# Kernel optimization log

Measured on AMD Instinct MI355X. Metric: run time of the kernel, lower is better.

The kernel has to match this reference:

```python
import jax, jax.numpy as jnp
import numpy as np
import math

B, S, H, NH, NB = 2, 512, 128, 4, 2
D = H // NH
V_ITEMS, NCAT, NMETA, BAG, TSPAN = 50000, 1000, 16, 5, 256
EPS_EMB, EPS = 1e-5, 1e-8
NEG = -(2.0 ** 32) + 1.0


def _ln(x, g, b, eps):
    m = x.mean(-1, keepdims=True)
    v = ((x - m) ** 2).mean(-1, keepdims=True)
    return (x - m) / jnp.sqrt(v + eps) * g + b


def setup_inputs() -> dict:
    key = jax.random.key(0)
    ks = jax.random.split(key, 24)
    sc = 0.02
    inp = {}
    inp['input_ids'] = jax.random.randint(ks[0], (B, S), 0, V_ITEMS + 1)
    inp['metadata_seq'] = jax.random.normal(ks[1], (B, S, NMETA), jnp.float32)
    inp['category_seq'] = jax.random.randint(ks[2], (B, S, BAG), 0, NCAT + 1)
    inp['time_matrix'] = jax.random.randint(ks[3], (B, S, S), 0, TSPAN + 1)
    item = jax.random.normal(ks[4], (V_ITEMS + 1, H), jnp.float32) * sc
    inp['item_emb_w'] = item.at[0].set(0.0)  # padding_idx=0 cleared
    cat = jax.random.normal(ks[5], (NCAT + 1, H // 2), jnp.float32) * sc
    inp['cat_emb_w'] = cat.at[0].set(0.0)
    inp['num_W'] = jax.random.normal(ks[6], (H // 2, NMETA), jnp.float32) * sc
    inp['num_b'] = jnp.zeros((H // 2,), jnp.float32)
    inp['fusion_W'] = jax.random.normal(ks[7], (H, 2 * H), jnp.float32) * sc
    inp['fusion_b'] = jnp.zeros((H,), jnp.float32)
    inp['emb_ln_g'] = jnp.ones((H,), jnp.float32)
    inp['emb_ln_b'] = jnp.zeros((H,), jnp.float32)
    inp['pos_K_w'] = jax.random.normal(ks[8], (S, H), jnp.float32) * sc
    inp['pos_V_w'] = jax.random.normal(ks[9], (S, H), jnp.float32) * sc
    inp['time_K_w'] = jax.random.normal(ks[10], (TSPAN + 1, H), jnp.float32) * sc
    inp['time_V_w'] = jax.random.normal(ks[11], (TSPAN + 1, H), jnp.float32) * sc
    inp['attn_ln_g'] = jnp.ones((NB, H), jnp.float32)
    inp['attn_ln_b'] = jnp.zeros((NB, H), jnp.float32)
    inp['Q_W'] = jax.random.normal(ks[12], (NB, H, H), jnp.float32) * sc
    inp['Q_b'] = jnp.zeros((NB, H), jnp.float32)
    inp['K_W'] = jax.random.normal(ks[13], (NB, H, H), jnp.float32) * sc
    inp['K_b'] = jnp.zeros((NB, H), jnp.float32)
    inp['V_W'] = jax.random.normal(ks[14], (NB, H, H), jnp.float32) * sc
    inp['V_b'] = jnp.zeros((NB, H), jnp.float32)
    inp['fwd_ln_g'] = jnp.ones((NB, H), jnp.float32)
    inp['fwd_ln_b'] = jnp.zeros((NB, H), jnp.float32)
    inp['w1_W'] = jax.random.normal(ks[15], (NB, H, H), jnp.float32) * sc
    inp['w1_b'] = jnp.zeros((NB, H), jnp.float32)
    inp['w2_W'] = jax.random.normal(ks[16], (NB, H, H), jnp.float32) * sc
    inp['w2_b'] = jnp.zeros((NB, H), jnp.float32)
    inp['last_ln_g'] = jnp.ones((H,), jnp.float32)
    inp['last_ln_b'] = jnp.zeros((H,), jnp.float32)
    return inp


def reference(input_ids, metadata_seq, category_seq, time_matrix, item_emb_w,
              cat_emb_w, num_W, num_b, fusion_W, fusion_b, emb_ln_g, emb_ln_b,
              pos_K_w, pos_V_w, time_K_w, time_V_w, attn_ln_g, attn_ln_b,
              Q_W, Q_b, K_W, K_b, V_W, V_b, fwd_ln_g, fwd_ln_b,
              w1_W, w1_b, w2_W, w2_b, last_ln_g, last_ln_b):
    # ---- seq2vec ----
    item_v = item_emb_w[input_ids] * math.sqrt(H)            # [B,S,H]
    bag_mask = (category_seq != 0)                           # EmbeddingBag mean, padding_idx=0
    cat_e = cat_emb_w[category_seq] * bag_mask[..., None]    # [B,S,BAG,H/2]
    cat_v = cat_e.sum(-2) / jnp.maximum(bag_mask.sum(-1, keepdims=True), 1)
    num_v = metadata_seq @ num_W.T + num_b                   # [B,S,H/2]
    comb = jnp.concatenate([item_v, num_v, cat_v], axis=-1)  # [B,S,2H]
    vecs = _ln(comb @ fusion_W.T + fusion_b, emb_ln_g, emb_ln_b, EPS_EMB)

    # ---- vec2feats ----
    posK = pos_K_w.reshape(S, NH, D)
    posV = pos_V_w.reshape(S, NH, D)
    tK = time_K_w[time_matrix].reshape(B, S, S, NH, D)       # [B,S,S,h,d]
    tV = time_V_w[time_matrix].reshape(B, S, S, NH, D)
    timeline = (input_ids == 0)                              # [B,S]
    keep = (~timeline)[..., None].astype(vecs.dtype)
    vecs = vecs * keep
    causal = ~jnp.tril(jnp.ones((S, S), bool))               # mask where j > i
    inv_sqrt_d = 1.0 / math.sqrt(D)

    for i in range(NB):
        Qn = _ln(vecs, attn_ln_g[i], attn_ln_b[i], EPS)
        Q = (Qn @ Q_W[i].T + Q_b[i]).reshape(B, S, NH, D)
        K = (vecs @ K_W[i].T + K_b[i]).reshape(B, S, NH, D)
        V = (vecs @ V_W[i].T + V_b[i]).reshape(B, S, NH, D)
        aw = jnp.einsum('bihd,bjhd->bhij', Q, K)
        aw = aw + jnp.einsum('bihd,jhd->bhij', Q, posK)
        aw = aw + jnp.einsum('bijhd,bihd->bhij', tK, Q)
        aw = aw * inv_sqrt_d
        aw = jnp.where(timeline[:, None, :, None], NEG, aw)  # masks query rows (as in torch)
        aw = jnp.where(causal[None, None], NEG, aw)
        aw = jax.nn.softmax(aw, axis=-1)
        out = jnp.einsum('bhij,bjhd->bihd', aw, V)
        out = out + jnp.einsum('bhij,jhd->bihd', aw, posV)
        out = out + jnp.einsum('bhij,bijhd->bihd', aw, tV)
        out = out.reshape(B, S, H)
        vecs = Qn + out
        vecs = _ln(vecs, fwd_ln_g[i], fwd_ln_b[i], EPS)
        h1 = jax.nn.gelu(vecs @ w1_W[i].T + w1_b[i], approximate=False)
        vecs = vecs + (h1 @ w2_W[i].T + w2_b[i])
        vecs = vecs * keep

    return _ln(vecs, last_ln_g, last_ln_b, EPS)
```

## Files before the change

kernel.cpp:

```cpp
#include <hip/hip_runtime.h>
#include <math.h>

#define Bn 2
#define Sn 512
#define Hn 128
#define NHn 4
#define Dn 32
#define BAGn 5
#define NMETAn 16
#define ROWS 1024
#define NBn 2
#define Tt 257

#define NEGF (-4294967295.0f)
#define INV_SQRT_D 0.17677669529663687f
#define SQRT_H 11.313708498984761f
#define EPS_EMB 1e-5f
#define EPSF 1e-8f

#define OFF_QN    0
#define OFF_Q     131072
#define OFF_K     262144
#define OFF_V     393216
#define OFF_O     524288

static __device__ __forceinline__ float red64(float v) {
#pragma unroll
    for (int m = 1; m < 64; m <<= 1) v += __shfl_xor(v, m, 64);
    return v;
}
static __device__ __forceinline__ float red64max(float v) {
#pragma unroll
    for (int m = 1; m < 64; m <<= 1) v = fmaxf(v, __shfl_xor(v, m, 64));
    return v;
}

__global__ __launch_bounds__(256) void embed_qkv_kernel(
    const int* __restrict__ ids, const float* __restrict__ meta,
    const int* __restrict__ cats,
    const float* __restrict__ item_w, const float* __restrict__ cat_w,
    const float* __restrict__ numW, const float* __restrict__ numb,
    const float* __restrict__ fusW, const float* __restrict__ fusb,
    const float* __restrict__ elng, const float* __restrict__ elnb,
    const float* __restrict__ alng, const float* __restrict__ alnb,
    const float* __restrict__ QW, const float* __restrict__ Qb,
    const float* __restrict__ KW, const float* __restrict__ Kb,
    const float* __restrict__ VW, const float* __restrict__ Vb,
    const float* __restrict__ posK, const float* __restrict__ posV,
    float* __restrict__ Qn, float* __restrict__ Q,
    float* __restrict__ K, float* __restrict__ V)
{
    int r0 = blockIdx.x * 2, t = threadIdx.x;
    __shared__ float combs[512], xs[256], qs[256], parts[256], pk[256], pv[256];
    __shared__ float wsum[8];
    __shared__ int idl[2];
    if (t < 2) idl[t] = ids[r0 + t];
    __syncthreads();
    { int r = t >> 7, c = t & 127; combs[r * 256 + c] = item_w[idl[r] * Hn + c] * SQRT_H; }
    if (t < 128) {
        int r = t >> 6, c = t & 63;
        float acc = numb[c];
#pragma unroll
        for (int m2 = 0; m2 < NMETAn; ++m2)
            acc += meta[(r0 + r) * NMETAn + m2] * numW[c * NMETAn + m2];
        combs[r * 256 + 128 + c] = acc;
    } else {
        int u = t - 128, r = u >> 6, c = u & 63;
        float ca = 0.f; int cnt = 0;
#pragma unroll
        for (int k2 = 0; k2 < BAGn; ++k2) {
            int cc2 = cats[(r0 + r) * BAGn + k2];
            if (cc2 != 0) { ca += cat_w[cc2 * 64 + c]; cnt++; }
        }
        combs[r * 256 + 192 + c] = ca / (float)(cnt > 0 ? cnt : 1);
    }
    __syncthreads();
    int h = t & 127, kh = t >> 7;
    {
        const float4* w4p = (const float4*)(fusW + h * 256 + kh * 128);
        const float* c0 = combs + kh * 128;
        const float* c1 = combs + 256 + kh * 128;
        float a0 = 0.f, a1 = 0.f, b0 = 0.f, b1 = 0.f;
#pragma unroll 16
        for (int k4 = 0; k4 < 32; ++k4) {
            float4 w4 = w4p[k4];
            int k = k4 * 4;
            a0 += c0[k] * w4.x + c0[k + 1] * w4.y;
            a1 += c0[k + 2] * w4.z + c0[k + 3] * w4.w;
            b0 += c1[k] * w4.x + c1[k + 1] * w4.y;
            b1 += c1[k + 2] * w4.z + c1[k + 3] * w4.w;
        }
        float A0 = a0 + a1, A1 = b0 + b1;
        if (kh) { parts[h] = A0; parts[128 + h] = A1; }
        __syncthreads();
        if (!kh) {
            xs[h] = A0 + parts[h] + fusb[h];
            xs[128 + h] = A1 + parts[128 + h] + fusb[h];
        }
    }
    __syncthreads();
    int w_ = t >> 6, row = w_ >> 1, l = t & 63, ch = ((w_ & 1) << 6) + l;
    float x = xs[row * 128 + ch];
    float s1 = red64(x);
    if (l == 0) wsum[w_] = s1;
    __syncthreads();
    float mean = (wsum[row * 2] + wsum[row * 2 + 1]) * (1.f / 128.f);
    float dlt = x - mean;
    float s2 = red64(dlt * dlt);
    if (l == 0) wsum[4 + w_] = s2;
    __syncthreads();
    float rstd = rsqrtf((wsum[4 + row * 2] + wsum[4 + row * 2 + 1]) * (1.f / 128.f) + EPS_EMB);
    float xv = dlt * rstd * elng[ch] + elnb[ch];
    xv = (idl[row] == 0) ? 0.f : xv;
    __syncthreads();
    xs[row * 128 + ch] = xv;
    __syncthreads();
    s1 = red64(xv);
    if (l == 0) wsum[w_] = s1;
    __syncthreads();
    mean = (wsum[row * 2] + wsum[row * 2 + 1]) * (1.f / 128.f);
    dlt = xv - mean;
    s2 = red64(dlt * dlt);
    if (l == 0) wsum[4 + w_] = s2;
    __syncthreads();
    rstd = rsqrtf((wsum[4 + row * 2] + wsum[4 + row * 2 + 1]) * (1.f / 128.f) + EPSF);
    float qn = dlt * rstd * alng[ch] + alnb[ch];
    qs[row * 128 + ch] = qn;
    Qn[(r0 + row) * 128 + ch] = qn;
    __syncthreads();
    {
        const float4* qw4 = (const float4*)(QW + h * 128 + kh * 64);
        const float4* kw4 = (const float4*)(KW + h * 128 + kh * 64);
        const float4* vw4 = (const float4*)(VW + h * 128 + kh * 64);
        const float* q0p = qs + kh * 64;
        const float* q1p = qs + 128 + kh * 64;
        const float* x0p = xs + kh * 64;
        const float* x1p = xs + 128 + kh * 64;
        float aq0 = 0, aq1 = 0, ak0 = 0, ak1 = 0, av0 = 0, av1 = 0;
#pragma unroll 8
        for (int k4 = 0; k4 < 16; ++k4) {
            float4 wq = qw4[k4], wk = kw4[k4], wv = vw4[k4];
            int k = k4 * 4;
            aq0 += q0p[k] * wq.x + q0p[k + 1] * wq.y + q0p[k + 2] * wq.z + q0p[k + 3] * wq.w;
            aq1 += q1p[k] * wq.x + q1p[k + 1] * wq.y + q1p[k + 2] * wq.z + q1p[k + 3] * wq.w;
            ak0 += x0p[k] * wk.x + x0p[k + 1] * wk.y + x0p[k + 2] * wk.z + x0p[k + 3] * wk.w;
            ak1 += x1p[k] * wk.x + x1p[k + 1] * wk.y + x1p[k + 2] * wk.z + x1p[k + 3] * wk.w;
            av0 += x0p[k] * wv.x + x0p[k + 1] * wv.y + x0p[k + 2] * wv.z + x0p[k + 3] * wv.w;
            av1 += x1p[k] * wv.x + x1p[k + 1] * wv.y + x1p[k + 2] * wv.z + x1p[k + 3] * wv.w;
        }
        if (kh) {
            parts[h] = aq0; parts[128 + h] = aq1;
            pk[h] = ak0; pk[128 + h] = ak1;
            pv[h] = av0; pv[128 + h] = av1;
        }
        __syncthreads();
        if (!kh) {
            int s0 = r0 & (Sn - 1), s1_ = (r0 + 1) & (Sn - 1);
            Q[r0 * 128 + h]       = aq0 + parts[h]       + Qb[h];
            Q[(r0 + 1) * 128 + h] = aq1 + parts[128 + h] + Qb[h];
            K[r0 * 128 + h]       = ak0 + pk[h]          + Kb[h] + posK[s0 * 128 + h];
            K[(r0 + 1) * 128 + h] = ak1 + pk[128 + h]    + Kb[h] + posK[s1_ * 128 + h];
            V[r0 * 128 + h]       = av0 + pv[h]          + Vb[h] + posV[s0 * 128 + h];
            V[(r0 + 1) * 128 + h] = av1 + pv[128 + h]    + Vb[h] + posV[s1_ * 128 + h];
        }
    }
}

static __device__ __forceinline__ void attn_phase(
    int b, int h, int i0, int t,
    const int* __restrict__ ids, const int* __restrict__ tmat,
    const float* __restrict__ Q, const float* __restrict__ K,
    const float* __restrict__ V,
    const float* __restrict__ tKw, const float* __restrict__ tVw,
    float* __restrict__ O,
    float* Kt, float* Vt, float* Stile, int* trowT,
    float* QTl, float* ql, int* tlf)
{
    if (t < 4) tlf[t] = (ids[b * Sn + i0 + t] == 0) ? 1 : 0;
    if (t < 128) {
        int q_ = t >> 5, d = t & 31;
        ql[q_ * 33 + d] = Q[(b * Sn + i0 + q_) * Hn + h * 32 + d];
    }
    __syncthreads();

    for (int tt = t; tt < Tt; tt += 256) {
        const float4* tk4 = (const float4*)(tKw + tt * Hn + h * 32);
        float a0 = 0.f, a1 = 0.f, a2 = 0.f, a3 = 0.f;
#pragma unroll
        for (int dv = 0; dv < 8; ++dv) {
            float4 w4 = tk4[dv];
            int d = dv * 4;
            a0 += ql[d] * w4.x + ql[d + 1] * w4.y + ql[d + 2] * w4.z + ql[d + 3] * w4.w;
            a1 += ql[33 + d] * w4.x + ql[34 + d] * w4.y + ql[35 + d] * w4.z + ql[36 + d] * w4.w;
            a2 += ql[66 + d] * w4.x + ql[67 + d] * w4.y + ql[68 + d] * w4.z + ql[69 + d] * w4.w;
            a3 += ql[99 + d] * w4.x + ql[100 + d] * w4.y + ql[101 + d] * w4.z + ql[102 + d] * w4.w;
        }
        QTl[tt] = a0; QTl[260 + tt] = a1; QTl[520 + tt] = a2; QTl[780 + tt] = a3;
    }

    int tl_any = tlf[0] | tlf[1] | tlf[2] | tlf[3];
    int ntiles = tl_any ? 8 : ((i0 + 3) >> 6) + 1;

    int iq = t >> 6, jj = t & 63;
    int i_g = i0 + iq;
    int my_tl = tlf[iq];
    const int* trow = tmat + (b * Sn + i_g) * Sn;

    float qreg[32];
#pragma unroll
    for (int d = 0; d < 32; ++d) qreg[d] = ql[iq * 33 + d];

    int jq = jj >> 5, d = jj & 31;
    float m = -INFINITY, lsum = 0.f, acc = 0.f;

    for (int jt = 0; jt < ntiles; ++jt) {
        int j0 = jt * 64;
        __syncthreads();
        for (int f = t; f < 64 * 8; f += 256) {
            int jl = f >> 3, dv = f & 7;
            const float* src = K + (b * Sn + j0 + jl) * Hn + h * 32 + dv * 4;
            float4 w4 = *(const float4*)src;
            float* kd = &Kt[jl * 33 + dv * 4];
            kd[0] = w4.x; kd[1] = w4.y; kd[2] = w4.z; kd[3] = w4.w;
            float4 v4 = *(const float4*)(V + (b * Sn + j0 + jl) * Hn + h * 32 + dv * 4);
            float* vd = &Vt[jl * 33 + dv * 4];
            vd[0] = v4.x; vd[1] = v4.y; vd[2] = v4.z; vd[3] = v4.w;
        }
        __syncthreads();

        int active = my_tl || (j0 <= i_g);
        if (active) {
            int j = j0 + jj;
            float sv = NEGF;
            int tv = trow[j];
            if (!my_tl && j <= i_g) {
                float a = 0.f;
#pragma unroll
                for (int dd = 0; dd < 32; ++dd)
                    a += qreg[dd] * Kt[jj * 33 + dd];
                sv = (a + QTl[iq * 260 + tv]) * INV_SQRT_D;
            }
            float mt = red64max(sv);
            float mnew = fmaxf(m, mt);
            float alpha = expf(m - mnew);
            float p = expf(sv - mnew);
            lsum = lsum * alpha + red64(p);
            m = mnew;
            acc *= alpha;
            Stile[iq * 64 + jj] = p;
            trowT[iq * 64 + jj] = tv;
        }
        __syncthreads();
        if (active) {
            int base = jq * 32;
#pragma unroll 8
            for (int jl = base; jl < base + 32; ++jl) {
                float pp = Stile[iq * 64 + jl];
                int tv2 = trowT[iq * 64 + jl];
                acc += pp * (Vt[jl * 33 + d] + tVw[tv2 * Hn + h * 32 + d]);
            }
        }
    }

    float a2 = acc + __shfl_xor(acc, 32, 64);
    if (jj < 32)
        O[(b * Sn + i_g) * Hn + h * 32 + d] = a2 / lsum;
}

__global__ __launch_bounds__(256) void attn_kernel(
    const int* ids, const int* tmat,
    const float* Q, const float* K, const float* V,
    const float* tKw, const float* tVw, float* O)
{
    __shared__ float Kt[64 * 33];
    __shared__ float Vt[64 * 33];
    __shared__ float Stile[4 * 64];
    __shared__ int   trowT[4 * 64];
    __shared__ float QTl[4 * 260];
    __shared__ float ql[4 * 33];
    __shared__ int tlf[4];
    int blk = blockIdx.x, t = threadIdx.x;
    int bh = blk & 7;
    int s  = blk >> 3;
    int g = s >> 5, r = s & 31;
    int m;
    if      (g == 0) m = r;
    else if (g == 1) m = 127 - r;
    else if (g == 2) m = 32 + r;
    else             m = 95 - r;
    int b = bh >> 2, h = bh & 3;
    attn_phase(b, h, m * 4, t, ids, tmat, Q, K, V, tKw, tVw, O,
               Kt, Vt, Stile, trowT, QTl, ql, tlf);
}

__global__ __launch_bounds__(256) void ffn_qkv_kernel(
    const int* __restrict__ ids, float* __restrict__ Qn,
    const float* __restrict__ O,
    const float* __restrict__ flng, const float* __restrict__ flnb,
    const float* __restrict__ w1W, const float* __restrict__ w1b,
    const float* __restrict__ w2W, const float* __restrict__ w2b,
    const float* __restrict__ alng, const float* __restrict__ alnb,
    const float* __restrict__ QW, const float* __restrict__ Qb,
    const float* __restrict__ KW, const float* __restrict__ Kb,
    const float* __restrict__ VW, const float* __restrict__ Vb,
    const float* __restrict__ posK, const float* __restrict__ posV,
    float* __restrict__ Q, float* __restrict__ K, float* __restrict__ V,
    const float* __restrict__ llng, const float* __restrict__ llnb,
    float* __restrict__ out, int nb, int last)
{
    int r0 = blockIdx.x * 2, t = threadIdx.x;
    __shared__ float ys[256], h1s[256], parts[256], pk[256], pv[256];
    __shared__ float wsum[8];
    ys[t] = Qn[r0 * 128 + t] + O[r0 * 128 + t];
    __syncthreads();
    int w_ = t >> 6, row = w_ >> 1, l = t & 63, ch = ((w_ & 1) << 6) + l;
    float x = ys[row * 128 + ch];
    float s1 = red64(x);
    if (l == 0) wsum[w_] = s1;
    __syncthreads();
    float mean = (wsum[row * 2] + wsum[row * 2 + 1]) * (1.f / 128.f);
    float dlt = x - mean;
    float s2 = red64(dlt * dlt);
    if (l == 0) wsum[4 + w_] = s2;
    __syncthreads();
    float rstd = rsqrtf((wsum[4 + row * 2] + wsum[4 + row * 2 + 1]) * (1.f / 128.f) + EPSF);
    float yv = dlt * rstd * flng[nb * 128 + ch] + flnb[nb * 128 + ch];
    __syncthreads();
    ys[row * 128 + ch] = yv;
    __syncthreads();

    int h = t & 127, kh = t >> 7;
    {
        const float4* w4p = (const float4*)(w1W + nb * 16384 + h * 128 + kh * 64);
        const float* y0 = ys + kh * 64;
        const float* y1 = ys + 128 + kh * 64;
        float a0 = 0.f, a1 = 0.f, b0 = 0.f, b1 = 0.f;
#pragma unroll 16
        for (int k4 = 0; k4 < 16; ++k4) {
            float4 w4 = w4p[k4];
            int k = k4 * 4;
            a0 += y0[k] * w4.x + y0[k + 1] * w4.y;
            a1 += y0[k + 2] * w4.z + y0[k + 3] * w4.w;
            b0 += y1[k] * w4.x + y1[k + 1] * w4.y;
            b1 += y1[k + 2] * w4.z + y1[k + 3] * w4.w;
        }
        float A0 = a0 + a1, A1 = b0 + b1;
        if (kh) { parts[h] = A0; parts[128 + h] = A1; }
        __syncthreads();
        if (!kh) {
            float v0 = A0 + parts[h] + w1b[nb * 128 + h];
            float v1 = A1 + parts[128 + h] + w1b[nb * 128 + h];
            h1s[h] = 0.5f * v0 * (1.f + erff(v0 * 0.70710678118654752f));
            h1s[128 + h] = 0.5f * v1 * (1.f + erff(v1 * 0.70710678118654752f));
        }
    }
    __syncthreads();
    {
        const float4* w4p = (const float4*)(w2W + nb * 16384 + h * 128 + kh * 64);
        const float* y0 = h1s + kh * 64;
        const float* y1 = h1s + 128 + kh * 64;
        float a0 = 0.f, a1 = 0.f, b0 = 0.f, b1 = 0.f;
#pragma unroll 16
        for (int k4 = 0; k4 < 16; ++k4) {
            float4 w4 = w4p[k4];
            int k = k4 * 4;
            a0 += y0[k] * w4.x + y0[k + 1] * w4.y;
            a1 += y0[k + 2] * w4.z + y0[k + 3] * w4.w;
            b0 += y1[k] * w4.x + y1[k + 1] * w4.y;
            b1 += y1[k + 2] * w4.z + y1[k + 3] * w4.w;
        }
        float A0 = a0 + a1, A1 = b0 + b1;
        __syncthreads();
        if (kh) { parts[h] = A0; parts[128 + h] = A1; }
        __syncthreads();
        if (!kh) {
            float z0 = A0 + parts[h] + w2b[nb * 128 + h] + ys[h];
            float z1 = A1 + parts[128 + h] + w2b[nb * 128 + h] + ys[128 + h];
            z0 = (ids[r0] == 0) ? 0.f : z0;
            z1 = (ids[r0 + 1] == 0) ? 0.f : z1;
            h1s[h] = z0; h1s[128 + h] = z1;
        }
    }
    __syncthreads();

    if (last) {
        x = h1s[row * 128 + ch];
        s1 = red64(x);
        if (l == 0) wsum[w_] = s1;
        __syncthreads();
        mean = (wsum[row * 2] + wsum[row * 2 + 1]) * (1.f / 128.f);
        dlt = x - mean;
        s2 = red64(dlt * dlt);
        if (l == 0) wsum[4 + w_] = s2;
        __syncthreads();
        rstd = rsqrtf((wsum[4 + row * 2] + wsum[4 + row * 2 + 1]) * (1.f / 128.f) + EPSF);
        out[(r0 + row) * 128 + ch] = dlt * rstd * llng[ch] + llnb[ch];
        return;
    }

    int nq = nb + 1;
    x = h1s[row * 128 + ch];
    s1 = red64(x);
    if (l == 0) wsum[w_] = s1;
    __syncthreads();
    mean = (wsum[row * 2] + wsum[row * 2 + 1]) * (1.f / 128.f);
    dlt = x - mean;
    s2 = red64(dlt * dlt);
    if (l == 0) wsum[4 + w_] = s2;
    __syncthreads();
    rstd = rsqrtf((wsum[4 + row * 2] + wsum[4 + row * 2 + 1]) * (1.f / 128.f) + EPSF);
    float qn = dlt * rstd * alng[nq * 128 + ch] + alnb[nq * 128 + ch];
    __syncthreads();
    ys[row * 128 + ch] = qn;
    Qn[(r0 + row) * 128 + ch] = qn;
    __syncthreads();

    {
        const float4* qw4 = (const float4*)(QW + nq * 16384 + h * 128 + kh * 64);
        const float4* kw4 = (const float4*)(KW + nq * 16384 + h * 128 + kh * 64);
        const float4* vw4 = (const float4*)(VW + nq * 16384 + h * 128 + kh * 64);
        const float* q0p = ys + kh * 64;
        const float* q1p = ys + 128 + kh * 64;
        const float* x0p = h1s + kh * 64;
        const float* x1p = h1s + 128 + kh * 64;
        float aq0 = 0, aq1 = 0, ak0 = 0, ak1 = 0, av0 = 0, av1 = 0;
#pragma unroll 8
        for (int k4 = 0; k4 < 16; ++k4) {
            float4 wq = qw4[k4], wk = kw4[k4], wv = vw4[k4];
            int k = k4 * 4;
            aq0 += q0p[k] * wq.x + q0p[k + 1] * wq.y + q0p[k + 2] * wq.z + q0p[k + 3] * wq.w;
            aq1 += q1p[k] * wq.x + q1p[k + 1] * wq.y + q1p[k + 2] * wq.z + q1p[k + 3] * wq.w;
            ak0 += x0p[k] * wk.x + x0p[k + 1] * wk.y + x0p[k + 2] * wk.z + x0p[k + 3] * wk.w;
            ak1 += x1p[k] * wk.x + x1p[k + 1] * wk.y + x1p[k + 2] * wk.z + x1p[k + 3] * wk.w;
            av0 += x0p[k] * wv.x + x0p[k + 1] * wv.y + x0p[k + 2] * wv.z + x0p[k + 3] * wv.w;
            av1 += x1p[k] * wv.x + x1p[k + 1] * wv.y + x1p[k + 2] * wv.z + x1p[k + 3] * wv.w;
        }
        if (kh) {
            parts[h] = aq0; parts[128 + h] = aq1;
            pk[h] = ak0; pk[128 + h] = ak1;
            pv[h] = av0; pv[128 + h] = av1;
        }
        __syncthreads();
        if (!kh) {
            int s0 = r0 & (Sn - 1), s1_ = (r0 + 1) & (Sn - 1);
            Q[r0 * 128 + h]       = aq0 + parts[h]       + Qb[nq * 128 + h];
            Q[(r0 + 1) * 128 + h] = aq1 + parts[128 + h] + Qb[nq * 128 + h];
            K[r0 * 128 + h]       = ak0 + pk[h]          + Kb[nq * 128 + h] + posK[s0 * 128 + h];
            K[(r0 + 1) * 128 + h] = ak1 + pk[128 + h]    + Kb[nq * 128 + h] + posK[s1_ * 128 + h];
            V[r0 * 128 + h]       = av0 + pv[h]          + Vb[nq * 128 + h] + posV[s0 * 128 + h];
            V[(r0 + 1) * 128 + h] = av1 + pv[128 + h]    + Vb[nq * 128 + h] + posV[s1_ * 128 + h];
        }
    }
}

extern "C" void kernel_launch(void* const* d_in, const int* in_sizes, int n_in,
                              void* d_out, int out_size, void* d_ws, size_t ws_size,
                              hipStream_t stream) {
    const int*   ids   = (const int*)  d_in[0];
    const float* meta  = (const float*)d_in[1];
    const int*   cats  = (const int*)  d_in[2];
    const int*   tmat  = (const int*)  d_in[3];
    const float* itemw = (const float*)d_in[4];
    const float* catw  = (const float*)d_in[5];
    const float* numW  = (const float*)d_in[6];
    const float* numb  = (const float*)d_in[7];
    const float* fusW  = (const float*)d_in[8];
    const float* fusb  = (const float*)d_in[9];
    const float* elng  = (const float*)d_in[10];
    const float* elnb  = (const float*)d_in[11];
    const float* posK  = (const float*)d_in[12];
    const float* posV  = (const float*)d_in[13];
    const float* tKw   = (const float*)d_in[14];
    const float* tVw   = (const float*)d_in[15];
    const float* alng  = (const float*)d_in[16];
    const float* alnb  = (const float*)d_in[17];
    const float* QW    = (const float*)d_in[18];
    const float* Qb    = (const float*)d_in[19];
    const float* KW    = (const float*)d_in[20];
    const float* Kb    = (const float*)d_in[21];
    const float* VW    = (const float*)d_in[22];
    const float* Vb    = (const float*)d_in[23];
    const float* flng  = (const float*)d_in[24];
    const float* flnb  = (const float*)d_in[25];
    const float* w1W   = (const float*)d_in[26];
    const float* w1b   = (const float*)d_in[27];
    const float* w2W   = (const float*)d_in[28];
    const float* w2b   = (const float*)d_in[29];
    const float* llng  = (const float*)d_in[30];
    const float* llnb  = (const float*)d_in[31];
    (void)in_sizes; (void)n_in; (void)out_size; (void)ws_size;

    float* ws = (float*)d_ws;
    float* Qn   = ws + OFF_QN;
    float* Q    = ws + OFF_Q;
    float* K    = ws + OFF_K;
    float* V    = ws + OFF_V;
    float* O    = ws + OFF_O;
    float* out  = (float*)d_out;

    embed_qkv_kernel<<<ROWS / 2, 256, 0, stream>>>(
        ids, meta, cats, itemw, catw, numW, numb, fusW, fusb, elng, elnb,
        alng, alnb, QW, Qb, KW, Kb, VW, Vb, posK, posV, Qn, Q, K, V);
    for (int nb = 0; nb < NBn; ++nb) {
        attn_kernel<<<1024, 256, 0, stream>>>(ids, tmat, Q, K, V, tKw, tVw, O);
        ffn_qkv_kernel<<<ROWS / 2, 256, 0, stream>>>(
            ids, Qn, O, flng, flnb, w1W, w1b, w2W, w2b,
            alng, alnb, QW, Qb, KW, Kb, VW, Vb, posK, posV,
            Q, K, V, llng, llnb, out, nb, (nb == NBn - 1) ? 1 : 0);
    }
}
```

Baseline: 263.7 us.

## Fuse embed, attention and FFN into one cooperative persistent kernel with grid syncs

Replaces the five separate launches (embed, then attention and FFN for each block) with a single cooperative kernel of 512 blocks. The stages are separated by grid-wide syncs, and shared memory is carved out of one buffer that all phases reuse. Each block handles two attention query tiles, pairing tile j with tile 127-j to balance the causal workload. This removes launch gaps and inter-kernel drain at the cost of grid-sync overhead and lower per-phase parallelism for attention (512 blocks instead of 1024). The old multi-kernel path is kept as a fallback when cooperative launch is unavailable.

```diff
diff --git a/kernel.cpp b/kernel.cpp
--- a/kernel.cpp
+++ b/kernel.cpp
@@ -1,5 +1,8 @@
 #include <hip/hip_runtime.h>
+#include <hip/hip_cooperative_groups.h>
 #include <math.h>
+
+namespace cg = cooperative_groups;
 
 #define Bn 2
 #define Sn 512
@@ -35,7 +38,8 @@
     return v;
 }
 
-__global__ __launch_bounds__(256) void embed_qkv_kernel(
+static __device__ __forceinline__ void embed2(
+    int r0, int t, float* sm,
     const int* __restrict__ ids, const float* __restrict__ meta,
     const int* __restrict__ cats,
     const float* __restrict__ item_w, const float* __restrict__ cat_w,
@@ -50,10 +54,15 @@
     float* __restrict__ Qn, float* __restrict__ Q,
     float* __restrict__ K, float* __restrict__ V)
 {
-    int r0 = blockIdx.x * 2, t = threadIdx.x;
-    __shared__ float combs[512], xs[256], qs[256], parts[256], pk[256], pv[256];
-    __shared__ float wsum[8];
-    __shared__ int idl[2];
+    float* combs = sm;
+    float* xs    = sm + 512;
+    float* qs    = sm + 768;
+    float* parts = sm + 1024;
+    float* pk    = sm + 1280;
+    float* pv    = sm + 1536;
+    float* wsum  = sm + 1792;
+    int*   idl   = (int*)(sm + 1800);
+
     if (t < 2) idl[t] = ids[r0 + t];
     __syncthreads();
     { int r = t >> 7, c = t & 127; combs[r * 256 + c] = item_w[idl[r] * Hn + c] * SQRT_H; }
@@ -176,6 +185,7 @@
     float* Kt, float* Vt, float* Stile, int* trowT,
     float* QTl, float* ql, int* tlf)
 {
+    __syncthreads();
     if (t < 4) tlf[t] = (ids[b * Sn + i0 + t] == 0) ? 1 : 0;
     if (t < 128) {
         int q_ = t >> 5, d = t & 31;
@@ -267,33 +277,8 @@
         O[(b * Sn + i_g) * Hn + h * 32 + d] = a2 / lsum;
 }
 
-__global__ __launch_bounds__(256) void attn_kernel(
-    const int* ids, const int* tmat,
-    const float* Q, const float* K, const float* V,
-    const float* tKw, const float* tVw, float* O)
-{
-    __shared__ float Kt[64 * 33];
-    __shared__ float Vt[64 * 33];
-    __shared__ float Stile[4 * 64];
-    __shared__ int   trowT[4 * 64];
-    __shared__ float QTl[4 * 260];
-    __shared__ float ql[4 * 33];
-    __shared__ int tlf[4];
-    int blk = blockIdx.x, t = threadIdx.x;
-    int bh = blk & 7;
-    int s  = blk >> 3;
-    int g = s >> 5, r = s & 31;
-    int m;
-    if      (g == 0) m = r;
-    else if (g == 1) m = 127 - r;
-    else if (g == 2) m = 32 + r;
-    else             m = 95 - r;
-    int b = bh >> 2, h = bh & 3;
-    attn_phase(b, h, m * 4, t, ids, tmat, Q, K, V, tKw, tVw, O,
-               Kt, Vt, Stile, trowT, QTl, ql, tlf);
-}
-
-__global__ __launch_bounds__(256) void ffn_qkv_kernel(
+static __device__ __forceinline__ void ffn2(
+    int r0, int t, float* sm,
     const int* __restrict__ ids, float* __restrict__ Qn,
     const float* __restrict__ O,
     const float* __restrict__ flng, const float* __restrict__ flnb,
@@ -308,9 +293,13 @@
     const float* __restrict__ llng, const float* __restrict__ llnb,
     float* __restrict__ out, int nb, int last)
 {
-    int r0 = blockIdx.x * 2, t = threadIdx.x;
-    __shared__ float ys[256], h1s[256], parts[256], pk[256], pv[256];
-    __shared__ float wsum[8];
+    float* ys    = sm;
+    float* h1s   = sm + 256;
+    float* parts = sm + 512;
+    float* pk    = sm + 768;
+    float* pv    = sm + 1024;
+    float* wsum  = sm + 1280;
+
     ys[t] = Qn[r0 * 128 + t] + O[r0 * 128 + t];
     __syncthreads();
     int w_ = t >> 6, row = w_ >> 1, l = t & 63, ch = ((w_ & 1) << 6) + l;
@@ -452,6 +441,106 @@
         }
     }
 }
+
+__global__ __launch_bounds__(256, 2) void fused_kernel(
+    const int* __restrict__ ids, const float* __restrict__ meta,
+    const int* __restrict__ cats, const int* __restrict__ tmat,
+    const float* __restrict__ item_w, const float* __restrict__ cat_w,
+    const float* __restrict__ numW, const float* __restrict__ numb,
+    const float* __restrict__ fusW, const float* __restrict__ fusb,
+    const float* __restrict__ elng, const float* __restrict__ elnb,
+    const float* __restrict__ posK, const float* __restrict__ posV,
+    const float* __restrict__ tKw, const float* __restrict__ tVw,
+    const float* __restrict__ alng, const float* __restrict__ alnb,
+    const float* __restrict__ QW, const float* __restrict__ Qb,
+    const float* __restrict__ KW, const float* __restrict__ Kb,
+    const float* __restrict__ VW, const float* __restrict__ Vb,
+    const float* __restrict__ flng, const float* __restrict__ flnb,
+    const float* __restrict__ w1W, const float* __restrict__ w1b,
+    const float* __restrict__ w2W, const float* __restrict__ w2b,
+    const float* __restrict__ llng, const float* __restrict__ llnb,
+    float* __restrict__ Qn, float* __restrict__ Q, float* __restrict__ K,
+    float* __restrict__ V, float* __restrict__ O, float* __restrict__ out)
+{
+    cg::grid_group grid = cg::this_grid();
+    __shared__ __align__(16) float sm[5912];
+    int blk = blockIdx.x, t = threadIdx.x;
+    int b8 = blk >> 6, j = blk & 63;
+    int ab = b8 >> 2, ah = b8 & 3;
+
+    embed2(blk * 2, t, sm, ids, meta, cats, item_w, cat_w, numW, numb,
+           fusW, fusb, elng, elnb, alng, alnb, QW, Qb, KW, Kb, VW, Vb,
+           posK, posV, Qn, Q, K, V);
+    grid.sync();
+
+    for (int nb = 0; nb < NBn; ++nb) {
+        attn_phase(ab, ah, j * 4, t, ids, tmat, Q, K, V, tKw, tVw, O,
+                   sm, sm + 2112, sm + 4224, (int*)(sm + 4480),
+                   sm + 4736, sm + 5776, (int*)(sm + 5908));
+        attn_phase(ab, ah, (127 - j) * 4, t, ids, tmat, Q, K, V, tKw, tVw, O,
+                   sm, sm + 2112, sm + 4224, (int*)(sm + 4480),
+                   sm + 4736, sm + 5776, (int*)(sm + 5908));
+        grid.sync();
+        ffn2(blk * 2, t, sm, ids, Qn, O, flng, flnb, w1W, w1b, w2W, w2b,
+             alng, alnb, QW, Qb, KW, Kb, VW, Vb, posK, posV,
+             Q, K, V, llng, llnb, out, nb, (nb == NBn - 1) ? 1 : 0);
+        if (nb == 0) grid.sync();
+    }
+}
+
+__global__ __launch_bounds__(256) void embed_qkv_kernel(
+    const int* ids, const float* meta, const int* cats,
+    const float* item_w, const float* cat_w, const float* numW, const float* numb,
+    const float* fusW, const float* fusb, const float* elng, const float* elnb,
+    const float* alng, const float* alnb,
+    const float* QW, const float* Qb, const float* KW, const float* Kb,
+    const float* VW, const float* Vb, const float* posK, const float* posV,
+    float* Qn, float* Q, float* K, float* V)
+{
+    __shared__ __align__(16) float sm[1802];
+    embed2(blockIdx.x * 2, threadIdx.x, sm, ids, meta, cats, item_w, cat_w,
+           numW, numb, fusW, fusb, elng, elnb, alng, alnb, QW, Qb, KW, Kb,
+           VW, Vb, posK, posV, Qn, Q, K, V);
+}
+
+__global__ __launch_bounds__(256) void attn_kernel(
+    const int* ids, const int* tmat,
+    const float* Q, const float* K, const float* V,
+    const float* tKw, const float* tVw, float* O)
+{
+    __shared__ __align__(16) float sm[5912];
+    int blk = blockIdx.x, t = threadIdx.x;
+    int bh = blk & 7;
+    int s  = blk >> 3;
+    int g = s >> 5, r = s & 31;
+    int mm;
+    if      (g == 0) mm = r;
+    else if (g == 1) mm = 127 - r;
+    else if (g == 2) mm = 32 + r;
+    else             mm = 95 - r;
+    int b = bh >> 2, h = bh & 3;
+    attn_phase(b, h, mm * 4, t, ids, tmat, Q, K, V, tKw, tVw, O,
+               sm, sm + 2112, sm + 4224, (int*)(sm + 4480),
+               sm + 4736, sm + 5776, (int*)(sm + 5908));
+}
+
+__global__ __launch_bounds__(256) void ffn_qkv_kernel(
+    const int* ids, float* Qn, const float* O,
+    const float* flng, const float* flnb,
+    const float* w1W, const float* w1b, const float* w2W, const float* w2b,
+    const float* alng, const float* alnb,
+    const float* QW, const float* Qb, const float* KW, const float* Kb,
+    const float* VW, const float* Vb, const float* posK, const float* posV,
+    float* Q, float* K, float* V,
+    const float* llng, const float* llnb, float* out, int nb, int last)
+{
+    __shared__ __align__(16) float sm[1288];
+    ffn2(blockIdx.x * 2, threadIdx.x, sm, ids, Qn, O, flng, flnb, w1W, w1b,
+         w2W, w2b, alng, alnb, QW, Qb, KW, Kb, VW, Vb, posK, posV,
+         Q, K, V, llng, llnb, out, nb, last);
+}
+
+static int g_mode = -1;
 
 extern "C" void kernel_launch(void* const* d_in, const int* in_sizes, int n_in,
                               void* d_out, int out_size, void* d_ws, size_t ws_size,
@@ -491,21 +580,54 @@
     (void)in_sizes; (void)n_in; (void)out_size; (void)ws_size;
 
     float* ws = (float*)d_ws;
-    float* Qn   = ws + OFF_QN;
-    float* Q    = ws + OFF_Q;
-    float* K    = ws + OFF_K;
-    float* V    = ws + OFF_V;
-    float* O    = ws + OFF_O;
-    float* out  = (float*)d_out;
+    float* Qnp = ws + OFF_QN;
+    float* Qp  = ws + OFF_Q;
+    float* Kp  = ws + OFF_K;
+    float* Vp  = ws + OFF_V;
+    float* Op  = ws + OFF_O;
+    float* outp = (float*)d_out;
+
+    if (g_mode < 0) {
+        int dev = 0;
+        (void)hipGetDevice(&dev);
+        int coop = 0;
+        (void)hipDeviceGetAttribute(&coop, hipDeviceAttributeCooperativeLaunch, dev);
+        int ncu = 0;
+        (void)hipDeviceGetAttribute(&ncu, hipDeviceAttributeMultiprocessorCount, dev);
+        int maxb = 0;
+        hipError_t oe = hipOccupancyMaxActiveBlocksPerMultiprocessor(
+            &maxb, fused_kernel, 256, 0);
+        g_mode = (coop && oe == hipSuccess && (long)maxb * (long)ncu >= 512) ? 1 : 0;
+    }
+
+    if (g_mode == 1) {
+        void* args[] = {
+            (void*)&ids, (void*)&meta, (void*)&cats, (void*)&tmat,
+            (void*)&itemw, (void*)&catw, (void*)&numW, (void*)&numb,
+            (void*)&fusW, (void*)&fusb, (void*)&elng, (void*)&elnb,
+            (void*)&posK, (void*)&posV, (void*)&tKw, (void*)&tVw,
+            (void*)&alng, (void*)&alnb, (void*)&QW, (void*)&Qb,
+            (void*)&KW, (void*)&Kb, (void*)&VW, (void*)&Vb,
+            (void*)&flng, (void*)&flnb, (void*)&w1W, (void*)&w1b,
+            (void*)&w2W, (void*)&w2b, (void*)&llng, (void*)&llnb,
+            (void*)&Qnp, (void*)&Qp, (void*)&Kp, (void*)&Vp, (void*)&Op,
+            (void*)&outp
+        };
+        hipError_t e = hipLaunchCooperativeKernel((void*)fused_kernel,
+                                                  dim3(512), dim3(256),
+                                                  args, 0, stream);
+        if (e == hipSuccess) return;
+        g_mode = 0;
+    }
 
     embed_qkv_kernel<<<ROWS / 2, 256, 0, stream>>>(
         ids, meta, cats, itemw, catw, numW, numb, fusW, fusb, elng, elnb,
-        alng, alnb, QW, Qb, KW, Kb, VW, Vb, posK, posV, Qn, Q, K, V);
+        alng, alnb, QW, Qb, KW, Kb, VW, Vb, posK, posV, Qnp, Qp, Kp, Vp);
     for (int nb = 0; nb < NBn; ++nb) {
-        attn_kernel<<<1024, 256, 0, stream>>>(ids, tmat, Q, K, V, tKw, tVw, O);
+        attn_kernel<<<1024, 256, 0, stream>>>(ids, tmat, Qp, Kp, Vp, tKw, tVw, Op);
         ffn_qkv_kernel<<<ROWS / 2, 256, 0, stream>>>(
-            ids, Qn, O, flng, flnb, w1W, w1b, w2W, w2b,
+            ids, Qnp, Op, flng, flnb, w1W, w1b, w2W, w2b,
             alng, alnb, QW, Qb, KW, Kb, VW, Vb, posK, posV,
-            Q, K, V, llng, llnb, out, nb, (nb == NBn - 1) ? 1 : 0);
-    }
-}
+            Qp, Kp, Vp, llng, llnb, outp, nb, (nb == NBn - 1) ? 1 : 0);
+    }
+}
```

Measured after the change: 258.5 us. 1.02x faster.
